# Kernel tuning notes

Measured on AMD Instinct MI355X. Metric: run time of the kernel, lower is better.

## Reference

```python
import jax, jax.numpy as jnp
import numpy as np

N_FEATURES = 1_000_000
N_FIELDS = 50
EMB_DIM = 64
ATT_DIM = EMB_DIM // 2
BATCH = 2048


def setup_inputs() -> dict:
    key = jax.random.key(0)
    ks = jax.random.split(key, 7)
    features = jax.random.randint(ks[0], (BATCH, N_FIELDS), 0, N_FEATURES)
    emb_table = jax.random.normal(ks[1], (N_FEATURES, EMB_DIM), dtype=jnp.float32) * 0.01
    coeff_table = jax.random.normal(ks[2], (N_FEATURES, 1), dtype=jnp.float32) * 0.01
    bias = jnp.zeros((1,), dtype=jnp.float32)
    # kaiming normal for relu: std = sqrt(2/fan_in)
    att_w = jax.random.normal(ks[3], (ATT_DIM, EMB_DIM), dtype=jnp.float32) * np.sqrt(2.0 / EMB_DIM)
    att_b = jnp.zeros((ATT_DIM,), dtype=jnp.float32)
    p = jax.random.normal(ks[4], (ATT_DIM, 1), dtype=jnp.float32)
    w = jnp.ones((EMB_DIM, 1), dtype=jnp.float32)
    return {"features": features, "emb_table": emb_table, "coeff_table": coeff_table,
            "bias": bias, "att_w": att_w, "att_b": att_b, "p": p, "w": w}


def reference(features, emb_table, coeff_table, bias, att_w, att_b, p, w):
    # Dropout layers in eval mode (identity).
    emb = emb_table[features]            # [B, F, D]
    coeff = coeff_table[features]        # [B, F, 1]
    iu, ju = jnp.triu_indices(N_FIELDS, k=1)
    # pairwise hadamard products in row-major (i,j) order matching the loop
    interactions = emb[:, iu, :] * emb[:, ju, :]   # [B, P, D], P = F*(F-1)/2
    # attention MLP: relu(x @ att_w^T + att_b) @ p -> scores over interactions
    hidden = jax.nn.relu(jnp.einsum('bpd,ad->bpa', interactions, att_w) + att_b)
    scores = jnp.einsum('bpa,ao->bpo', hidden, p)  # [B, P, 1]
    att = jax.nn.softmax(scores, axis=1)           # softmax over interaction dim
    pooled = jnp.sum(interactions * att, axis=1)   # [B, D]
    interaction_part = (pooled @ w).reshape(-1)    # [B]
    linear_part = jnp.sum(coeff, axis=1).reshape(-1)
    return interaction_part + linear_part + bias
```

## Files before the change

kernel.cpp:

```cpp
#include <hip/hip_runtime.h>
#include <hip/hip_fp16.h>
#include <math.h>

#define NFIELDS 50
#define EMBD 64
#define NPAIRS 1225
#define NTILEPAD 40
#define NPAD (NTILEPAD * 32)
#define NSEQ 4
#define NWAVES 4
#define NITER 10
#define NTHREADS 256
#define NFPAD 51
#define CHSTR (NFPAD * 8)

typedef _Float16 f16x8 __attribute__((ext_vector_type(8)));
typedef _Float16 f16x2 __attribute__((ext_vector_type(2)));
typedef __fp16   fp16x2 __attribute__((ext_vector_type(2)));
typedef float f32x16 __attribute__((ext_vector_type(16)));

union F16x8U { f16x8 v; f16x2 h2[4]; unsigned int u[4]; uint4 q; };
union U32F { unsigned int u; f16x2 h; fp16x2 g; };

__device__ __forceinline__ f16x2 pkrtz(float a, float b) {
    U32F t; t.g = __builtin_amdgcn_cvt_pkrtz(a, b);
    return t.h;
}

__device__ __forceinline__ f16x2 pkmax0(f16x2 a) {
#if __has_builtin(__builtin_elementwise_max)
    f16x2 z; z[0] = (_Float16)0; z[1] = (_Float16)0;
    return __builtin_elementwise_max(a, z);
#else
    f16x2 r;
    r[0] = a[0] > (_Float16)0 ? a[0] : (_Float16)0;
    r[1] = a[1] > (_Float16)0 ? a[1] : (_Float16)0;
    return r;
#endif
}

__launch_bounds__(NTHREADS, 3)
__global__ void afm_kernel(const int* __restrict__ features,
                           const float* __restrict__ emb_table,
                           const float* __restrict__ coeff_table,
                           const float* __restrict__ bias,
                           const float* __restrict__ att_w,
                           const float* __restrict__ att_b,
                           const float* __restrict__ pvec,
                           const float* __restrict__ wvec,
                           float* __restrict__ out)
{
    __shared__ __align__(16) unsigned short emb3[2][8][NFPAD][8];
    __shared__ unsigned short pair_s[NPAD];
    __shared__ int   feat_s[NSEQ][NFIELDS];
    __shared__ float red_s[2][NWAVES], red_st[2][NWAVES];
    __shared__ float csum_s[NSEQ];

    const int b0   = blockIdx.x * NSEQ;
    const int tid  = threadIdx.x;
    const int lane = tid & 63;
    const int wid  = tid >> 6;
    const int col  = lane & 31;
    const int h    = lane >> 5;
    const int h4   = h * 4;

    {
        float cacc = 0.f;
        if (lane < NFIELDS) {
            const int f = features[(b0 + wid) * NFIELDS + lane];
            feat_s[wid][lane] = f;
            cacc = coeff_table[f];
        } else if (lane == NFIELDS) {
            cacc = bias[0];
        }
        #pragma unroll
        for (int m = 1; m < 64; m <<= 1) cacc += __shfl_xor(cacc, m, 64);
        if (lane == 0) csum_s[wid] = cacc;
    }

    #pragma unroll
    for (int k = 0; k < NPAD / NTHREADS; ++k) {
        const int q = tid + k * NTHREADS;
        int i = 0, j = 1;
        if (q < NPAIRS) {
            const float s = sqrtf((float)(9801 - 8 * q));
            i = (int)((99.0f - s) * 0.5f);
            const int off = i * NFIELDS - ((i * (i + 1)) >> 1);
            j = i + 1 + (q - off);
        }
        pair_s[q] = (unsigned short)((i << 8) | j);
    }

    f16x8 afragW[4];
    f16x2 w2[16];
    #pragma unroll
    for (int c = 0; c < 4; ++c) {
        const int d0 = c * 16 + h * 8;
        const float4 wa0 = *reinterpret_cast<const float4*>(&att_w[col * EMBD + d0]);
        const float4 wa1 = *reinterpret_cast<const float4*>(&att_w[col * EMBD + d0 + 4]);
        F16x8U bf;
        bf.v[0] = (_Float16)wa0.x; bf.v[1] = (_Float16)wa0.y;
        bf.v[2] = (_Float16)wa0.z; bf.v[3] = (_Float16)wa0.w;
        bf.v[4] = (_Float16)wa1.x; bf.v[5] = (_Float16)wa1.y;
        bf.v[6] = (_Float16)wa1.z; bf.v[7] = (_Float16)wa1.w;
        afragW[c] = bf.v;
        const float4 wv0 = *reinterpret_cast<const float4*>(&wvec[d0]);
        const float4 wv1 = *reinterpret_cast<const float4*>(&wvec[d0 + 4]);
        f16x2 t0; t0[0] = (_Float16)wv0.x; t0[1] = (_Float16)wv0.y; w2[c * 4 + 0] = t0;
        f16x2 t1; t1[0] = (_Float16)wv0.z; t1[1] = (_Float16)wv0.w; w2[c * 4 + 1] = t1;
        f16x2 t2; t2[0] = (_Float16)wv1.x; t2[1] = (_Float16)wv1.y; w2[c * 4 + 2] = t2;
        f16x2 t3; t3[0] = (_Float16)wv1.z; t3[1] = (_Float16)wv1.w; w2[c * 4 + 3] = t3;
    }
    float attb_r[16];
    f16x2 p16[8];
    #pragma unroll
    for (int q = 0; q < 4; ++q) {
        const float4 ab = *reinterpret_cast<const float4*>(&att_b[8 * q + 4 * h]);
        attb_r[4 * q + 0] = ab.x; attb_r[4 * q + 1] = ab.y;
        attb_r[4 * q + 2] = ab.z; attb_r[4 * q + 3] = ab.w;
        const float4 pp = *reinterpret_cast<const float4*>(&pvec[8 * q + 4 * h]);
        f16x2 pa; pa[0] = (_Float16)pp.x; pa[1] = (_Float16)pp.y; p16[2 * q]     = pa;
        f16x2 pb; pb[0] = (_Float16)pp.z; pb[1] = (_Float16)pp.w; p16[2 * q + 1] = pb;
    }
    __syncthreads();

    float4 greg[4];

#define GISSUE(ee)                                                          \
    {                                                                       \
        _Pragma("unroll")                                                   \
        for (int k = 0; k < 4; ++k) {                                       \
            const int idx = tid + k * NTHREADS;                             \
            if (idx < NFIELDS * 16) {                                       \
                const int f  = idx >> 4;                                    \
                const int d0 = (idx & 15) * 4;                              \
                greg[k] = *reinterpret_cast<const float4*>(                 \
                    &emb_table[(size_t)feat_s[ee][f] * EMBD + d0]);         \
            }                                                               \
        }                                                                   \
    }

#define GWRITE(buf)                                                         \
    {                                                                       \
        _Pragma("unroll")                                                   \
        for (int k = 0; k < 4; ++k) {                                       \
            const int idx = tid + k * NTHREADS;                             \
            if (idx < NFIELDS * 16) {                                       \
                const int f  = idx >> 4;                                    \
                const int d0 = (idx & 15) * 4;                              \
                const int c  = d0 >> 4;                                     \
                const int hh = (d0 >> 3) & 1;                               \
                const int e0 = d0 & 7;                                      \
                U32F t0, t1;                                                \
                t0.h[0] = (_Float16)greg[k].x; t0.h[1] = (_Float16)greg[k].y; \
                t1.h[0] = (_Float16)greg[k].z; t1.h[1] = (_Float16)greg[k].w; \
                uint2 pk; pk.x = t0.u; pk.y = t1.u;                         \
                *reinterpret_cast<uint2*>(&emb3[buf][hh * 4 + c][f][e0]) = pk; \
            }                                                               \
        }                                                                   \
    }

    GISSUE(0);
    GWRITE(0);
    __syncthreads();

    #pragma unroll 1
    for (int e = 0; e < NSEQ; ++e) {
        if (e + 1 < NSEQ) GISSUE(e + 1);

        const unsigned short* const ebase =
            &emb3[e & 1][0][0][0] + h4 * CHSTR;
        float s_run = 0.f, st_run = 0.f;

        #pragma unroll 2
        for (int tt = 0; tt < NITER; ++tt) {
            const int tile = wid + tt * NWAVES;
            const int q    = tile * 32 + col;
            const unsigned int ij = pair_s[q];
            const int fi = ij >> 8;
            const int fj = ij & 255;

            const unsigned short* pi = ebase + fi * 8;
            const unsigned short* pj = ebase + fj * 8;

            f32x16 acc;
            #pragma unroll
            for (int reg = 0; reg < 16; ++reg) acc[reg] = attb_r[reg];

            f16x2 th2; th2[0] = (_Float16)0; th2[1] = (_Float16)0;
            #pragma unroll
            for (int c = 0; c < 4; ++c) {
                F16x8U ai, aj;
                ai.q = *reinterpret_cast<const uint4*>(pi + c * CHSTR);
                aj.q = *reinterpret_cast<const uint4*>(pj + c * CHSTR);
                const f16x2 x0 = ai.h2[0] * aj.h2[0];
                const f16x2 x1 = ai.h2[1] * aj.h2[1];
                const f16x2 x2 = ai.h2[2] * aj.h2[2];
                const f16x2 x3 = ai.h2[3] * aj.h2[3];
                th2 = x0 * w2[c * 4 + 0] + th2;
                th2 = x1 * w2[c * 4 + 1] + th2;
                th2 = x2 * w2[c * 4 + 2] + th2;
                th2 = x3 * w2[c * 4 + 3] + th2;
                F16x8U bf;
                bf.h2[0] = x0; bf.h2[1] = x1; bf.h2[2] = x2; bf.h2[3] = x3;
                acc = __builtin_amdgcn_mfma_f32_32x32x16_f16(afragW[c], bf.v, acc, 0, 0, 0);
            }

            f16x2 sp2; sp2[0] = (_Float16)0; sp2[1] = (_Float16)0;
            #pragma unroll
            for (int qq = 0; qq < 8; ++qq) {
                const f16x2 av = pkmax0(pkrtz(acc[2 * qq], acc[2 * qq + 1]));
                sp2 = av * p16[qq] + sp2;
            }
            const float sp     = (float)sp2[0] + (float)sp2[1];
            const float t_half = (float)th2[0] + (float)th2[1];

            U32F pkd, oth;
            pkd.h = pkrtz(sp, t_half);
            oth.u = (unsigned int)__shfl_xor((int)pkd.u, 32, 64);
            const float sc = sp + (float)oth.h[0];
            const float tf = t_half + (float)oth.h[1];

            const float ex = (q < NPAIRS) ? __expf(sc) : 0.f;
            s_run  += ex;
            st_run += ex * tf;
        }

        #pragma unroll
        for (int m = 1; m < 64; m <<= 1) {
            s_run  += __shfl_xor(s_run, m, 64);
            st_run += __shfl_xor(st_run, m, 64);
        }
        if (lane == 0) { red_s[e & 1][wid] = s_run; red_st[e & 1][wid] = st_run; }

        if (e + 1 < NSEQ) GWRITE((e + 1) & 1);
        __syncthreads();

        if (tid == 0) {
            const float S  = red_s[e & 1][0] + red_s[e & 1][1]
                           + red_s[e & 1][2] + red_s[e & 1][3];
            const float ST = red_st[e & 1][0] + red_st[e & 1][1]
                           + red_st[e & 1][2] + red_st[e & 1][3];
            out[b0 + e] = ST / S + csum_s[e];
        }
    }

#undef GISSUE
#undef GWRITE
}

extern "C" void kernel_launch(void* const* d_in, const int* in_sizes, int n_in,
                              void* d_out, int out_size, void* d_ws, size_t ws_size,
                              hipStream_t stream) {
    const int*   features    = (const int*)d_in[0];
    const float* emb_table   = (const float*)d_in[1];
    const float* coeff_table = (const float*)d_in[2];
    const float* bias        = (const float*)d_in[3];
    const float* att_w       = (const float*)d_in[4];
    const float* att_b       = (const float*)d_in[5];
    const float* pvec        = (const float*)d_in[6];
    const float* wvec        = (const float*)d_in[7];
    float* out = (float*)d_out;

    const int batch = in_sizes[0] / NFIELDS;
    afm_kernel<<<batch / NSEQ, NTHREADS, 0, stream>>>(
        features, emb_table, coeff_table, bias, att_w, att_b, pvec, wvec, out);
}
```

Before: 29.81 us.

## Pack two independent sequence groups into one 512-thread block

```diff
diff --git a/kernel.cpp b/kernel.cpp
--- a/kernel.cpp
+++ b/kernel.cpp
@@ -7,10 +7,11 @@
 #define NPAIRS 1225
 #define NTILEPAD 40
 #define NPAD (NTILEPAD * 32)
+#define NGRP 2
 #define NSEQ 4
 #define NWAVES 4
 #define NITER 10
-#define NTHREADS 256
+#define NTHREADS 512
 #define NFPAD 51
 #define CHSTR (NFPAD * 8)
 
@@ -39,7 +40,7 @@
 #endif
 }
 
-__launch_bounds__(NTHREADS, 3)
+__launch_bounds__(NTHREADS, 2)
 __global__ void afm_kernel(const int* __restrict__ features,
                            const float* __restrict__ emb_table,
                            const float* __restrict__ coeff_table,
@@ -50,19 +51,22 @@
                            const float* __restrict__ wvec,
                            float* __restrict__ out)
 {
-    __shared__ __align__(16) unsigned short emb3[2][8][NFPAD][8];
+    __shared__ __align__(16) unsigned short emb3[NGRP][2][8][NFPAD][8];
     __shared__ unsigned short pair_s[NPAD];
-    __shared__ int   feat_s[NSEQ][NFIELDS];
-    __shared__ float red_s[2][NWAVES], red_st[2][NWAVES];
-    __shared__ float csum_s[NSEQ];
-
-    const int b0   = blockIdx.x * NSEQ;
+    __shared__ int   feat_s[NGRP * NSEQ][NFIELDS];
+    __shared__ float red_s[NGRP][2][NWAVES], red_st[NGRP][2][NWAVES];
+    __shared__ float csum_s[NGRP * NSEQ];
+
+    const int b0   = blockIdx.x * (NGRP * NSEQ);
     const int tid  = threadIdx.x;
     const int lane = tid & 63;
     const int wid  = tid >> 6;
+    const int grp  = wid >> 2;
+    const int wg   = wid & 3;
     const int col  = lane & 31;
     const int h    = lane >> 5;
     const int h4   = h * 4;
+    const int tg   = tid & 255;
 
     {
         float cacc = 0.f;
@@ -79,16 +83,18 @@
     }
 
     #pragma unroll
-    for (int k = 0; k < NPAD / NTHREADS; ++k) {
+    for (int k = 0; k < 3; ++k) {
         const int q = tid + k * NTHREADS;
-        int i = 0, j = 1;
-        if (q < NPAIRS) {
-            const float s = sqrtf((float)(9801 - 8 * q));
-            i = (int)((99.0f - s) * 0.5f);
-            const int off = i * NFIELDS - ((i * (i + 1)) >> 1);
-            j = i + 1 + (q - off);
-        }
-        pair_s[q] = (unsigned short)((i << 8) | j);
+        if (q < NPAD) {
+            int i = 0, j = 1;
+            if (q < NPAIRS) {
+                const float s = sqrtf((float)(9801 - 8 * q));
+                i = (int)((99.0f - s) * 0.5f);
+                const int off = i * NFIELDS - ((i * (i + 1)) >> 1);
+                j = i + 1 + (q - off);
+            }
+            pair_s[q] = (unsigned short)((i << 8) | j);
+        }
     }
 
     f16x8 afragW[4];
@@ -126,16 +132,16 @@
 
     float4 greg[4];
 
-#define GISSUE(ee)                                                          \
+#define GISSUE(ei)                                                          \
     {                                                                       \
         _Pragma("unroll")                                                   \
         for (int k = 0; k < 4; ++k) {                                       \
-            const int idx = tid + k * NTHREADS;                             \
+            const int idx = tg + k * 256;                                   \
             if (idx < NFIELDS * 16) {                                       \
                 const int f  = idx >> 4;                                    \
                 const int d0 = (idx & 15) * 4;                              \
                 greg[k] = *reinterpret_cast<const float4*>(                 \
-                    &emb_table[(size_t)feat_s[ee][f] * EMBD + d0]);         \
+                    &emb_table[(size_t)feat_s[ei][f] * EMBD + d0]);         \
             }                                                               \
         }                                                                   \
     }
@@ -144,7 +150,7 @@
     {                                                                       \
         _Pragma("unroll")                                                   \
         for (int k = 0; k < 4; ++k) {                                       \
-            const int idx = tid + k * NTHREADS;                             \
+            const int idx = tg + k * 256;                                   \
             if (idx < NFIELDS * 16) {                                       \
                 const int f  = idx >> 4;                                    \
                 const int d0 = (idx & 15) * 4;                              \
@@ -155,26 +161,27 @@
                 t0.h[0] = (_Float16)greg[k].x; t0.h[1] = (_Float16)greg[k].y; \
                 t1.h[0] = (_Float16)greg[k].z; t1.h[1] = (_Float16)greg[k].w; \
                 uint2 pk; pk.x = t0.u; pk.y = t1.u;                         \
-                *reinterpret_cast<uint2*>(&emb3[buf][hh * 4 + c][f][e0]) = pk; \
+                *reinterpret_cast<uint2*>(&emb3[grp][buf][hh * 4 + c][f][e0]) = pk; \
             }                                                               \
         }                                                                   \
     }
 
-    GISSUE(0);
+    GISSUE(grp * NSEQ + 0);
     GWRITE(0);
     __syncthreads();
 
     #pragma unroll 1
     for (int e = 0; e < NSEQ; ++e) {
-        if (e + 1 < NSEQ) GISSUE(e + 1);
+        const int ei = grp * NSEQ + e;
+        if (e + 1 < NSEQ) GISSUE(ei + 1);
 
         const unsigned short* const ebase =
-            &emb3[e & 1][0][0][0] + h4 * CHSTR;
+            &emb3[grp][e & 1][0][0][0] + h4 * CHSTR;
         float s_run = 0.f, st_run = 0.f;
 
         #pragma unroll 2
         for (int tt = 0; tt < NITER; ++tt) {
-            const int tile = wid + tt * NWAVES;
+            const int tile = wg + tt * NWAVES;
             const int q    = tile * 32 + col;
             const unsigned int ij = pair_s[q];
             const int fi = ij >> 8;
@@ -231,17 +238,17 @@
             s_run  += __shfl_xor(s_run, m, 64);
             st_run += __shfl_xor(st_run, m, 64);
         }
-        if (lane == 0) { red_s[e & 1][wid] = s_run; red_st[e & 1][wid] = st_run; }
+        if (lane == 0) { red_s[grp][e & 1][wg] = s_run; red_st[grp][e & 1][wg] = st_run; }
 
         if (e + 1 < NSEQ) GWRITE((e + 1) & 1);
         __syncthreads();
 
-        if (tid == 0) {
-            const float S  = red_s[e & 1][0] + red_s[e & 1][1]
-                           + red_s[e & 1][2] + red_s[e & 1][3];
-            const float ST = red_st[e & 1][0] + red_st[e & 1][1]
-                           + red_st[e & 1][2] + red_st[e & 1][3];
-            out[b0 + e] = ST / S + csum_s[e];
+        if (tg == 0) {
+            const float S  = red_s[grp][e & 1][0] + red_s[grp][e & 1][1]
+                           + red_s[grp][e & 1][2] + red_s[grp][e & 1][3];
+            const float ST = red_st[grp][e & 1][0] + red_st[grp][e & 1][1]
+                           + red_st[grp][e & 1][2] + red_st[grp][e & 1][3];
+            out[b0 + ei] = ST / S + csum_s[ei];
         }
     }
 
@@ -263,6 +270,6 @@
     float* out = (float*)d_out;
 
     const int batch = in_sizes[0] / NFIELDS;
-    afm_kernel<<<batch / NSEQ, NTHREADS, 0, stream>>>(
+    afm_kernel<<<batch / (NGRP * NSEQ), NTHREADS, 0, stream>>>(
         features, emb_table, coeff_table, bias, att_w, att_b, pvec, wvec, out);
 }
```

New measurement: 30.04 us. About the same (+0.8%).
